# Kernel optimization log

Measured on AMD Instinct MI355X. Metric: run time of the kernel, lower is better.

## Reference

```python
import jax, jax.numpy as jnp
import numpy as np

L, Q = 256, 21
LAMBDA_H = 1e-06
LAMBDA_J = 0.0001
M = 8192


def setup_inputs() -> dict:
    key = jax.random.key(0)
    k1, k2, k3, k4 = jax.random.split(key, 4)
    seqs = jax.random.randint(k1, (M, L), 0, Q, dtype=jnp.int64 if jax.config.jax_enable_x64 else jnp.int32)
    weights = jax.random.uniform(k2, (M,), dtype=jnp.float32)
    h = jax.random.normal(k3, (L, Q), dtype=jnp.float32) * 0.1
    J = jax.random.normal(k4, (L, L, Q, Q), dtype=jnp.float32) * 0.02
    return {"seqs": seqs, "weights": weights, "h": h, "J": J}


def reference(seqs, weights, h, J):
    # strictly-lower-triangular mask over (i, j): j < i
    tril = jnp.tril(jnp.ones((L, L), dtype=bool), k=-1)
    Jm = J * tril[:, :, None, None]                       # (L, L, q, q)

    # one-hot history; H[b, j, k] = 1 iff seqs[b, j] == k
    H = jax.nn.one_hot(seqs, Q, dtype=h.dtype)            # (M, L, q)

    # contrib[b, i, a] = sum_{j<i, k} J[i, j, a, k] * H[b, j, k]
    # == one big (M, L*q) x (L*q, L*q) causal-masked matmul
    contrib = jnp.einsum('ijak,bjk->bia', Jm, H)          # (M, L, q)

    logits = h[None, :, :] + contrib                      # (M, L, q)
    logp = jax.nn.log_softmax(logits, axis=-1)            # (M, L, q)

    # gather label log-probs
    ll = jnp.take_along_axis(logp, seqs[..., None], axis=-1)[..., 0]  # (M, L)

    M_eff = jnp.maximum(weights.sum(), 1e-12)
    w_norm = weights / M_eff
    nll = -(w_norm[:, None] * ll).sum()

    reg_h = 0.5 * LAMBDA_H * jnp.sum(h ** 2)
    reg_J = 0.5 * LAMBDA_J * jnp.sum(Jm ** 2)
    loss = nll + reg_h + reg_J
    return (loss, nll, reg_h + reg_J)
```

## Files before the change

kernel.cpp:

```cpp
#include <hip/hip_runtime.h>
#include <cstdint>
#include <cstddef>

#define L_   256
#define Q_   21
#define M_   8192
#define QQ   441
#define JCH  16
#define SCALE    32.0f
#define INVSCALE 0.03125f
#define NPAIR ((L_ * (L_ - 1)) / 2)


#define NPREPT 4080
#define GPREP  (NPREPT + 256 + 2)

typedef _Float16 h2 __attribute__((ext_vector_type(2)));
typedef float    f32x4 __attribute__((ext_vector_type(4)));
typedef unsigned u32x4 __attribute__((ext_vector_type(4)));

__device__ __forceinline__ float block_reduce_sum(float v) {
    __shared__ float s[256];
    int t = threadIdx.x;
    __syncthreads();
    s[t] = v;
    __syncthreads();
#pragma unroll
    for (int o = 128; o > 0; o >>= 1) {
        if (t < o) s[t] += s[t + o];
        __syncthreads();
    }
    return s[0];
}

__global__ __launch_bounds__(256) void k_prep(const float* __restrict__ J,
                                              const int* __restrict__ seqs,
                                              const float* __restrict__ w,
                                              const float* __restrict__ h,
                                              unsigned* __restrict__ Jt,
                                              unsigned* __restrict__ seqsP,
                                              float* __restrict__ acc2,
                                              float* __restrict__ scal) {
    const int bid = blockIdx.x;
    const int t = threadIdx.x;

    if (bid < NPREPT) {
        __shared__ __align__(16) float sB[16 * QQ];
        const int i  = (bid >> 4) + 1;
        const int j0 = (bid & 15) << 4;
        if (j0 >= i) {
            if (t == 0) acc2[bid] = 0.f;
            return;
        }
        const int jn = min(16, i - j0);

        const float* src = J + (size_t)(i * L_ + j0) * QQ;
        const int ndw = jn * QQ;
        const int nf4 = ndw >> 2;
        const int rem = ndw & 3;

        float v2 = 0.f;
        {
            const f32x4* src4 = reinterpret_cast<const f32x4*>(src);
            f32x4* s4 = reinterpret_cast<f32x4*>(sB);
            for (int q = t; q < nf4; q += 256) {
                f32x4 v = __builtin_nontemporal_load(src4 + q);
                s4[q] = v;
                v2 += v.x * v.x + v.y * v.y + v.z * v.z + v.w * v.w;
            }
            if (t < rem) {
                float v = src[(nf4 << 2) + t];
                sB[(nf4 << 2) + t] = v;
                v2 += v * v;
            }
        }
        __syncthreads();

        {
            const int tri = i * (i - 1) / 2;
            const int nu4 = jn << 6;
            u32x4* dst = reinterpret_cast<u32x4*>(Jt + (size_t)(tri + j0) * 256);
            for (int g = t; g < nu4; g += 256) {
                const float* s = sB + (g >> 6) * QQ;
                unsigned wv[4];
#pragma unroll
                for (int c = 0; c < 4; ++c) {
                    const int dd = ((g & 63) << 2) | c;
                    const int kr = dd / 12;
                    const int dw = dd - 12 * kr;
                    const int a0 = dw << 1;
                    unsigned outw = 0;
                    if (kr < Q_) {
                        float x0 = (a0     < Q_) ? s[(a0    ) * Q_ + kr] : 0.f;
                        float x1 = (a0 + 1 < Q_) ? s[(a0 + 1) * Q_ + kr] : 0.f;
                        union { _Float16 hh[2]; unsigned u; } uu;
                        uu.hh[0] = (_Float16)(x0 * SCALE);
                        uu.hh[1] = (_Float16)(x1 * SCALE);
                        outw = uu.u;
                    }
                    wv[c] = outw;
                }
                u32x4 o;
                o.x = wv[0]; o.y = wv[1]; o.z = wv[2]; o.w = wv[3];
                __builtin_nontemporal_store(o, dst + g);
            }
        }

        float r = block_reduce_sum(v2);
        if (t == 0) acc2[bid] = r;
    } else if (bid < NPREPT + 256) {
        const int u  = bid - NPREPT;
        const int b  = ((u >> 3) << 8) + t;
        const int jc = u & 7;
        const int4* row = reinterpret_cast<const int4*>(seqs + (size_t)b * L_);
#pragma unroll
        for (int u8 = 0; u8 < 8; ++u8) {
            const int jq = jc * 8 + u8;
            int4 v = row[jq];
            unsigned p = (unsigned)(v.x & 255) | ((unsigned)(v.y & 255) << 8) |
                         ((unsigned)(v.z & 255) << 16) | ((unsigned)(v.w & 255) << 24);
            seqsP[jq * M_ + b] = p;
        }
    } else if (bid == NPREPT + 256) {
        float v = 0.f;
        for (int x = t; x < M_; x += 256) v += w[x];
        float r = block_reduce_sum(v);
        if (t == 0) scal[0] = r;
    } else {
        float v2 = 0.f;
        for (int x = t; x < L_ * Q_; x += 256) { float y = h[x]; v2 += y * y; }
        float r2 = block_reduce_sum(v2);
        if (t == 0) scal[1] = r2;
    }
}

#define BODY(jj)                                                                    \
    {                                                                               \
        const unsigned kk = (idxw[(jj) >> 2] >> (((jj) & 3) * 8)) & 255u;           \
        const uint4* rp = reinterpret_cast<const uint4*>(sJ) + ((jj) * 64 + kk * 3);\
        union { uint4 u; h2 h[4]; } ra, rb, rc;                                     \
        ra.u = rp[0]; rb.u = rp[1]; rc.u = rp[2];                                   \
        acch[0]  += ra.h[0]; acch[1]  += ra.h[1];                                   \
        acch[2]  += ra.h[2]; acch[3]  += ra.h[3];                                   \
        acch[4]  += rb.h[0]; acch[5]  += rb.h[1];                                   \
        acch[6]  += rb.h[2]; acch[7]  += rb.h[3];                                   \
        acch[8]  += rc.h[0]; acch[9]  += rc.h[1];                                   \
        acch[10] += rc.h[2]; acch[11] += rc.h[3];                                   \
    }

__global__ __launch_bounds__(256, 8) void k_main(const unsigned* __restrict__ Jt,
                                                 const float* __restrict__ h,
                                                 const unsigned* __restrict__ seqsP,
                                                 const float* __restrict__ weights,
                                                 float* __restrict__ accL) {
    __shared__ unsigned sJ[JCH * 256];

    const int bid = blockIdx.x;
    const int i = (L_ - 1) - (bid >> 5);
    const int b = ((bid & 31) << 8) + threadIdx.x;

    h2 acch[12];
    const float* hp = h + i * Q_;
#pragma unroll
    for (int m = 0; m < 10; ++m) {
        acch[m].x = (_Float16)(hp[2 * m] * SCALE);
        acch[m].y = (_Float16)(hp[2 * m + 1] * SCALE);
    }
    acch[10].x = (_Float16)(hp[20] * SCALE); acch[10].y = (_Float16)0.f;
    acch[11].x = (_Float16)0.f;              acch[11].y = (_Float16)0.f;

    const unsigned* Jrow = Jt + (size_t)(i * (i - 1) / 2) * 256;
    const int nStages = i >> 4;
    const int rem     = i & 15;

    for (int s = 0; s < nStages; ++s) {
        const int j0 = s << 4;
        {
            const uint4* src = reinterpret_cast<const uint4*>(Jrow + j0 * 256);
            uint4* dst = reinterpret_cast<uint4*>(sJ);
#pragma unroll
            for (int n = 0; n < 4; ++n) {
                dst[n * 256 + threadIdx.x] = src[n * 256 + threadIdx.x];
            }
        }
        __syncthreads();

        unsigned idxw[JCH / 4];
#pragma unroll
        for (int q = 0; q < JCH / 4; ++q) {
            idxw[q] = seqsP[((j0 >> 2) + q) * M_ + b];
        }

#pragma unroll
        for (int jj = 0; jj < JCH; ++jj) BODY(jj);

        __syncthreads();
    }

    if (rem) {
        const int j0 = nStages << 4;
        {
            const uint4* src = reinterpret_cast<const uint4*>(Jrow + j0 * 256);
            uint4* dst = reinterpret_cast<uint4*>(sJ);
#pragma unroll
            for (int n = 0; n < 4; ++n) {
                dst[n * 256 + threadIdx.x] = src[n * 256 + threadIdx.x];
            }
        }
        __syncthreads();

        unsigned idxw[JCH / 4];
#pragma unroll
        for (int q = 0; q < JCH / 4; ++q) {
            idxw[q] = seqsP[((j0 >> 2) + q) * M_ + b];
        }

#pragma unroll
        for (int jj = 0; jj < JCH; ++jj) {
            if (jj >= rem) break;
            BODY(jj);
        }
    }

    float l[21];
#pragma unroll
    for (int m = 0; m < 10; ++m) {
        l[2 * m]     = (float)acch[m].x * INVSCALE;
        l[2 * m + 1] = (float)acch[m].y * INVSCALE;
    }
    l[20] = (float)acch[10].x * INVSCALE;

    unsigned lw = seqsP[(i >> 2) * M_ + b];
    int lbl = (int)((lw >> ((i & 3) * 8)) & 255u);

    float m = l[0];
#pragma unroll
    for (int a = 1; a < 21; ++a) m = fmaxf(m, l[a]);
    float s = 0.f;
    float lv = l[0];
#pragma unroll
    for (int a = 0; a < 21; ++a) {
        s += __expf(l[a] - m);
        if (a > 0) lv = (a == lbl) ? l[a] : lv;
    }
    float ll = (lv - m) - __logf(s);
    float contrib = weights[b] * ll;

    float r = block_reduce_sum(contrib);
    if (threadIdx.x == 0) accL[bid] = r;
}

__global__ __launch_bounds__(256) void k_final(const float* __restrict__ acc2,
                                               const float* __restrict__ accL,
                                               const float* __restrict__ scal,
                                               float* __restrict__ out) {
    int t = threadIdx.x;
    float j2 = 0.f;
    for (int x = t; x < NPREPT; x += 256) j2 += acc2[x];
    j2 = block_reduce_sum(j2);
    float lls = 0.f;
    for (int x = t; x < M_; x += 256) lls += accL[x];
    lls = block_reduce_sum(lls);
    if (t == 0) {
        float wsum = fmaxf(scal[0], 1e-12f);
        float nll = -lls / wsum;
        float reg = 0.5e-6f * scal[1] + 0.5e-4f * j2;
        out[0] = nll + reg;
        out[1] = nll;
        out[2] = reg;
    }
}

extern "C" void kernel_launch(void* const* d_in, const int* in_sizes, int n_in,
                              void* d_out, int out_size, void* d_ws, size_t ws_size,
                              hipStream_t stream) {
    const int*   seqs    = (const int*)d_in[0];
    const float* weights = (const float*)d_in[1];
    const float* h       = (const float*)d_in[2];
    const float* J       = (const float*)d_in[3];
    float* out = (float*)d_out;

    char* ws = (char*)d_ws;
    float*    acc2  = (float*)ws;
    float*    accL  = (float*)(ws + 16384);
    float*    scal  = (float*)(ws + 49152);
    unsigned* seqsP = (unsigned*)(ws + 65536);
    unsigned* Jt    = (unsigned*)(ws + 65536 + (size_t)(L_ / 4) * M_ * sizeof(unsigned));


    k_prep<<<GPREP, 256, 0, stream>>>(J, seqs, weights, h, Jt, seqsP, acc2, scal);
    k_main<<<L_ * (M_ / 256), 256, 0, stream>>>(Jt, h, seqsP, weights, accL);
    k_final<<<1, 256, 0, stream>>>(acc2, accL, scal, out);
}
```

Baseline: 387.6 us.

## Shrink prep tiles to 8 pairs with per-wave staging and split main into two launches

The prep kernel now handles 8 (i,j) pairs per block instead of 16. Each wave stages two pairs in its own LDS region and transposes them to fp16 with one 16-byte store per lane, which doubles the grid and cuts LDS use per block. The main kernel is launched twice, once for even and once for odd row offsets, with accumulator slots and workspace offsets widened to match. This aims to improve occupancy and load balance in prep and to interleave long and short rows in main, at the cost of an extra launch and more small blocks.

```diff
diff --git a/kernel.cpp b/kernel.cpp
--- a/kernel.cpp
+++ b/kernel.cpp
@@ -12,11 +12,10 @@
 #define NPAIR ((L_ * (L_ - 1)) / 2)
 
 
-#define NPREPT 4080
+#define NPREPT 8160
 #define GPREP  (NPREPT + 256 + 2)
 
 typedef _Float16 h2 __attribute__((ext_vector_type(2)));
-typedef float    f32x4 __attribute__((ext_vector_type(4)));
 typedef unsigned u32x4 __attribute__((ext_vector_type(4)));
 
 __device__ __forceinline__ float block_reduce_sum(float v) {
@@ -45,65 +44,62 @@
     const int t = threadIdx.x;
 
     if (bid < NPREPT) {
-        __shared__ __align__(16) float sB[16 * QQ];
-        const int i  = (bid >> 4) + 1;
-        const int j0 = (bid & 15) << 4;
+        __shared__ __align__(16) float sB[4 * 2 * 448];
+        const int i  = (bid >> 5) + 1;
+        const int j0 = (bid & 31) << 3;
         if (j0 >= i) {
             if (t == 0) acc2[bid] = 0.f;
             return;
         }
-        const int jn = min(16, i - j0);
-
-        const float* src = J + (size_t)(i * L_ + j0) * QQ;
-        const int ndw = jn * QQ;
-        const int nf4 = ndw >> 2;
-        const int rem = ndw & 3;
+        const int jn = min(8, i - j0);
+        const int wv = t >> 6;
+        const int l  = t & 63;
+        const int p0 = wv << 1;
+        const int pn = min(2, jn - p0);
+        float* sW = sB + wv * (2 * 448);
 
         float v2 = 0.f;
-        {
-            const f32x4* src4 = reinterpret_cast<const f32x4*>(src);
-            f32x4* s4 = reinterpret_cast<f32x4*>(sB);
-            for (int q = t; q < nf4; q += 256) {
-                f32x4 v = __builtin_nontemporal_load(src4 + q);
-                s4[q] = v;
-                v2 += v.x * v.x + v.y * v.y + v.z * v.z + v.w * v.w;
-            }
-            if (t < rem) {
-                float v = src[(nf4 << 2) + t];
-                sB[(nf4 << 2) + t] = v;
-                v2 += v * v;
-            }
-        }
-        __syncthreads();
-
-        {
-            const int tri = i * (i - 1) / 2;
-            const int nu4 = jn << 6;
-            u32x4* dst = reinterpret_cast<u32x4*>(Jt + (size_t)(tri + j0) * 256);
-            for (int g = t; g < nu4; g += 256) {
-                const float* s = sB + (g >> 6) * QQ;
-                unsigned wv[4];
-#pragma unroll
-                for (int c = 0; c < 4; ++c) {
-                    const int dd = ((g & 63) << 2) | c;
-                    const int kr = dd / 12;
-                    const int dw = dd - 12 * kr;
-                    const int a0 = dw << 1;
-                    unsigned outw = 0;
-                    if (kr < Q_) {
-                        float x0 = (a0     < Q_) ? s[(a0    ) * Q_ + kr] : 0.f;
-                        float x1 = (a0 + 1 < Q_) ? s[(a0 + 1) * Q_ + kr] : 0.f;
-                        union { _Float16 hh[2]; unsigned u; } uu;
-                        uu.hh[0] = (_Float16)(x0 * SCALE);
-                        uu.hh[1] = (_Float16)(x1 * SCALE);
-                        outw = uu.u;
-                    }
-                    wv[c] = outw;
+        for (int pp = 0; pp < pn; ++pp) {
+            const float* src = J + (size_t)(i * L_ + j0 + p0 + pp) * QQ;
+            float* d = sW + pp * 448;
+#pragma unroll
+            for (int r = 0; r < 7; ++r) {
+                const int idx = (r << 6) + l;
+                if (idx < QQ) {
+                    float v = __builtin_nontemporal_load(src + idx);
+                    d[idx] = v;
+                    v2 += v * v;
                 }
-                u32x4 o;
-                o.x = wv[0]; o.y = wv[1]; o.z = wv[2]; o.w = wv[3];
-                __builtin_nontemporal_store(o, dst + g);
-            }
+            }
+        }
+        __syncthreads();
+
+        const int tri = i * (i - 1) / 2;
+        for (int pp = 0; pp < pn; ++pp) {
+            const float* s = sW + pp * 448;
+            u32x4* dst = reinterpret_cast<u32x4*>(
+                Jt + (size_t)(tri + j0 + p0 + pp) * 256);
+            unsigned wvv[4];
+#pragma unroll
+            for (int c = 0; c < 4; ++c) {
+                const int dd = (l << 2) | c;
+                const int kr = dd / 12;
+                const int dw = dd - 12 * kr;
+                const int a0 = dw << 1;
+                unsigned outw = 0;
+                if (kr < Q_) {
+                    float x0 = (a0     < Q_) ? s[(a0    ) * Q_ + kr] : 0.f;
+                    float x1 = (a0 + 1 < Q_) ? s[(a0 + 1) * Q_ + kr] : 0.f;
+                    union { _Float16 hh[2]; unsigned u; } uu;
+                    uu.hh[0] = (_Float16)(x0 * SCALE);
+                    uu.hh[1] = (_Float16)(x1 * SCALE);
+                    outw = uu.u;
+                }
+                wvv[c] = outw;
+            }
+            u32x4 o;
+            o.x = wvv[0]; o.y = wvv[1]; o.z = wvv[2]; o.w = wvv[3];
+            __builtin_nontemporal_store(o, dst + l);
         }
 
         float r = block_reduce_sum(v2);
@@ -152,11 +148,13 @@
                                                  const float* __restrict__ h,
                                                  const unsigned* __restrict__ seqsP,
                                                  const float* __restrict__ weights,
-                                                 float* __restrict__ accL) {
+                                                 float* __restrict__ accL,
+                                                 const int ibase) {
     __shared__ unsigned sJ[JCH * 256];
 
     const int bid = blockIdx.x;
-    const int i = (L_ - 1) - (bid >> 5);
+    const int ii = ((bid >> 5) << 1) | ibase;
+    const int i = (L_ - 1) - ii;
     const int b = ((bid & 31) << 8) + threadIdx.x;
 
     h2 acch[12];
@@ -247,7 +245,7 @@
     float contrib = weights[b] * ll;
 
     float r = block_reduce_sum(contrib);
-    if (threadIdx.x == 0) accL[bid] = r;
+    if (threadIdx.x == 0) accL[(ibase << 12) + bid] = r;
 }
 
 __global__ __launch_bounds__(256) void k_final(const float* __restrict__ acc2,
@@ -282,13 +280,14 @@
 
     char* ws = (char*)d_ws;
     float*    acc2  = (float*)ws;
-    float*    accL  = (float*)(ws + 16384);
-    float*    scal  = (float*)(ws + 49152);
-    unsigned* seqsP = (unsigned*)(ws + 65536);
-    unsigned* Jt    = (unsigned*)(ws + 65536 + (size_t)(L_ / 4) * M_ * sizeof(unsigned));
+    float*    accL  = (float*)(ws + 32768);
+    float*    scal  = (float*)(ws + 65536);
+    unsigned* seqsP = (unsigned*)(ws + 131072);
+    unsigned* Jt    = (unsigned*)(ws + 131072 + (size_t)(L_ / 4) * M_ * sizeof(unsigned));
 
 
     k_prep<<<GPREP, 256, 0, stream>>>(J, seqs, weights, h, Jt, seqsP, acc2, scal);
-    k_main<<<L_ * (M_ / 256), 256, 0, stream>>>(Jt, h, seqsP, weights, accL);
+    k_main<<<4096, 256, 0, stream>>>(Jt, h, seqsP, weights, accL, 0);
+    k_main<<<4096, 256, 0, stream>>>(Jt, h, seqsP, weights, accL, 1);
     k_final<<<1, 256, 0, stream>>>(acc2, accL, scal, out);
 }
```

After: 395.9 us. 1.02x slower.
